# Performance work log

Measured on AMD Instinct MI355X. Metric: run time of the kernel, lower is better.

The kernel has to match this reference:

```python
import jax, jax.numpy as jnp
import numpy as np

B, T, D_IN, H, D_OUT = 64, 512, 256, 1024, 256


def _gru_cell(x, h, Wi, Wh, bi, bh):
    # x: [B, in_dim], h: [B, H]; Wi: [3H, in_dim], Wh: [3H, H]
    gi = x @ Wi.T + bi  # [B, 3H]
    gh = h @ Wh.T + bh  # [B, 3H]
    i_r, i_z, i_n = jnp.split(gi, 3, axis=-1)
    h_r, h_z, h_n = jnp.split(gh, 3, axis=-1)
    r = jax.nn.sigmoid(i_r + h_r)
    z = jax.nn.sigmoid(i_z + h_z)
    n = jnp.tanh(i_n + r * h_n)
    return (1.0 - z) * n + z * h


def setup_inputs() -> dict:
    key = jax.random.key(0)
    ks = jax.random.split(key, 11)
    s_in = 1.0 / np.sqrt(D_IN)
    s_h = 1.0 / np.sqrt(H)
    return {
        "x": jax.random.normal(ks[0], (B, T, D_IN), jnp.float32),
        "Wi0": jax.random.normal(ks[1], (3 * H, D_IN), jnp.float32) * s_in,
        "Wh0": jax.random.normal(ks[2], (3 * H, H), jnp.float32) * s_h,
        "bi0": jax.random.normal(ks[3], (3 * H,), jnp.float32) * s_h,
        "bh0": jax.random.normal(ks[4], (3 * H,), jnp.float32) * s_h,
        "Wi1": jax.random.normal(ks[5], (3 * H, H), jnp.float32) * s_h,
        "Wh1": jax.random.normal(ks[6], (3 * H, H), jnp.float32) * s_h,
        "bi1": jax.random.normal(ks[7], (3 * H,), jnp.float32) * s_h,
        "bh1": jax.random.normal(ks[8], (3 * H,), jnp.float32) * s_h,
        "Wo": jax.random.normal(ks[9], (D_OUT, H), jnp.float32) * s_h,
        "bo": jax.random.normal(ks[10], (D_OUT,), jnp.float32) * s_h,
    }


def reference(x, Wi0, Wh0, bi0, bh0, Wi1, Wh1, bi1, bh1, Wo, bo):
    b = x.shape[0]
    h0 = jnp.zeros((b, H), x.dtype)
    h1 = jnp.zeros((b, H), x.dtype)

    def step(carry, x_t):
        h0, h1 = carry
        h0 = _gru_cell(x_t, h0, Wi0, Wh0, bi0, bh0)
        h1 = _gru_cell(h0, h1, Wi1, Wh1, bi1, bh1)
        return (h0, h1), None

    (h0, h1), _ = jax.lax.scan(step, (h0, h1), jnp.swapaxes(x, 0, 1))
    return h1 @ Wo.T + bo  # [B, D_OUT]
```

## Files before the change

### kernel.cpp

```cpp
#include <hip/hip_runtime.h>

constexpr int kB    = 64;
constexpr int kT    = 512;
constexpr int kDin  = 256;
constexpr int kH    = 1024;
constexpr int kH3   = 3072;
constexpr int kDout = 256;
constexpr int kHB   = kB * kH;

typedef float  f32x4  __attribute__((ext_vector_type(4)));
typedef __bf16 bf16x8 __attribute__((ext_vector_type(8)));
typedef unsigned u32x4 __attribute__((ext_vector_type(4)));
typedef unsigned long long u64;

__device__ __forceinline__ float b2f(unsigned short u) {
  union { float f; unsigned u32; } c; c.u32 = ((unsigned)u) << 16; return c.f;
}
__device__ __forceinline__ unsigned short f2b(float f) {
  union { float f; unsigned u32; } c; c.f = f;
  unsigned r = c.u32 + 0x7fffu + ((c.u32 >> 16) & 1u);
  return (unsigned short)(r >> 16);
}
__device__ __forceinline__ bf16x8 ld8(const unsigned short* p) {
  return *reinterpret_cast<const bf16x8*>(p);
}
__device__ __forceinline__ u64 ald(const u64* p) {
  return __hip_atomic_load(p, __ATOMIC_RELAXED, __HIP_MEMORY_SCOPE_AGENT);
}
__device__ __forceinline__ unsigned ald32(const unsigned* p) {
  return __hip_atomic_load(p, __ATOMIC_RELAXED, __HIP_MEMORY_SCOPE_AGENT);
}
__device__ __forceinline__ void ast32(unsigned* p, unsigned v) {
  __hip_atomic_store(p, v, __ATOMIC_RELAXED, __HIP_MEMORY_SCOPE_AGENT);
}
__device__ __forceinline__ float sigm_(float x) { return 1.f / (1.f + __expf(-x)); }
__device__ __forceinline__ float tanh_(float x) {
  return 1.f - 2.f / (__expf(2.f * x) + 1.f);
}

#define MFMA16(a, b, c) __builtin_amdgcn_mfma_f32_16x16x32_bf16((a), (b), (c), 0, 0, 0)

__device__ __forceinline__ int swzcol(int C, int quad) {
  return (C & ~63) + ((quad ^ (((C >> 3) ^ (C >> 6)) & 7)) << 3);
}

__device__ __forceinline__ void stage_seg(unsigned short* ldsrow,
                                          const unsigned short* src, int s,
                                          int rmode) {
  if (rmode) {
    u32x4 d[8];
#pragma unroll
    for (int i = 0; i < 8; ++i) d[i] = *(const u32x4*)(src + i * 8);
#pragma unroll
    for (int i = 0; i < 8; ++i)
      *(u32x4*)&ldsrow[s * 64 + ((i ^ s) & 7) * 8] = d[i];
  } else {
    u64 w[16];
#pragma unroll
    for (int i = 0; i < 16; ++i) w[i] = ald((const u64*)src + i);
#pragma unroll
    for (int i = 0; i < 16; ++i)
      *(u64*)&ldsrow[s * 64 + (((i >> 1) ^ s) & 7) * 8 + (i & 1) * 4] = w[i];
  }
}

__device__ __forceinline__ void stage_half(unsigned short (*hl)[1032],
                                           const unsigned short* rbase,
                                           int kh, int lane, int rmode) {
  const int r = lane >> 2;
  const int s = kh * 8 + (lane & 3) * 2;
  const unsigned short* src = rbase + (size_t)r * kH + s * 64;
  stage_seg(hl[r], src, s, rmode);
  stage_seg(hl[r], src + 64, s + 1, rmode);
}

__device__ __forceinline__ void pb_post(unsigned* p, unsigned v, int lane) {
  if (lane == 0)
    __hip_atomic_store(p, v, __ATOMIC_RELEASE, __HIP_MEMORY_SCOPE_WORKGROUP);
}
__device__ __forceinline__ void pb_wait(unsigned* p, unsigned v) {
  while (__hip_atomic_load(p, __ATOMIC_ACQUIRE, __HIP_MEMORY_SCOPE_WORKGROUP) < v)
    __builtin_amdgcn_s_sleep(1);
}

__global__ void gru_prep(const float* __restrict__ x,
                         const float* __restrict__ Wi0, const float* __restrict__ Wh0,
                         const float* __restrict__ bi0, const float* __restrict__ bh0,
                         const float* __restrict__ Wi1, const float* __restrict__ Wh1,
                         const float* __restrict__ bi1, const float* __restrict__ bh1,
                         unsigned short* __restrict__ xb,
                         unsigned short* __restrict__ wi0b, unsigned short* __restrict__ wh0b,
                         unsigned short* __restrict__ wi1b, unsigned short* __restrict__ wh1b,
                         unsigned short* __restrict__ r0, unsigned short* __restrict__ r1,
                         float* __restrict__ bias, unsigned* __restrict__ sync) {
  const int stride = gridDim.x * blockDim.x;
  const int g = blockIdx.x * blockDim.x + threadIdx.x;
  for (int i = g; i < kH3 * kDin; i += stride) wi0b[i] = f2b(Wi0[i]);
  for (int i = g; i < kH3 * kH; i += stride) {
    wh0b[i] = f2b(Wh0[i]); wi1b[i] = f2b(Wi1[i]); wh1b[i] = f2b(Wh1[i]);
  }
  for (int i = g; i < kB * kT * kDin; i += stride) xb[i] = f2b(x[i]);
  for (int i = g; i < kHB; i += stride) { r0[i] = 0; r1[i] = 0; }
  for (int i = g; i < kH; i += stride) {
    bias[0 * kH + i] = bi0[0 * kH + i] + bh0[0 * kH + i];
    bias[1 * kH + i] = bi0[1 * kH + i] + bh0[1 * kH + i];
    bias[2 * kH + i] = bi0[2 * kH + i];
    bias[3 * kH + i] = bh0[2 * kH + i];
    bias[4 * kH + i] = bi1[0 * kH + i] + bh1[0 * kH + i];
    bias[5 * kH + i] = bi1[1 * kH + i] + bh1[1 * kH + i];
    bias[6 * kH + i] = bi1[2 * kH + i];
    bias[7 * kH + i] = bh1[2 * kH + i];
  }
  for (int i = g; i < 4096; i += stride) sync[i] = 0;
}

__global__ void __launch_bounds__(256, 1) gru_main(
    const unsigned short* __restrict__ xb,
    const unsigned short* __restrict__ wi0, const unsigned short* __restrict__ wh0,
    const unsigned short* __restrict__ wi1, const unsigned short* __restrict__ wh1,
    const float* __restrict__ bias,
    unsigned short* __restrict__ r0, unsigned short* __restrict__ r1,
    unsigned* __restrict__ sync, const int rmode,
    const float* __restrict__ Wo, const float* __restrict__ bo,
    float* __restrict__ out) {
  __shared__ unsigned short hl0[16][1032];
  __shared__ unsigned short hl1[16][1032];
  __shared__ float red[2][4][64][5];
  __shared__ bf16x8 wlds[2][32][64];
  __shared__ unsigned pb[8];

  const int tid  = threadIdx.x;
  const int lane = tid & 63;
  const int wv   = tid >> 6;
  const int ln15 = lane & 15;
  const int quad = lane >> 4;

  const int xcd   = blockIdx.x & 7;
  const int rest  = blockIdx.x >> 3;
  const int jsub  = rest & 7;
  const int mtile = rest >> 3;
  const int pidx  = xcd * 8 + jsub;

  const int layer = wv >> 1;
  const int kh    = wv & 1;
  const int jrow  = xcd * 128 + jsub * 16 + ln15;
  const int jcol  = jrow;

  const unsigned short *pw_r, *pw_z, *pw_n, *pv_r, *pv_z, *pv_n;
  if (layer == 0) {
    pw_r = wh0 + (size_t)(0 * kH + jrow) * kH + kh * 512 + quad * 8;
    pw_z = wh0 + (size_t)(1 * kH + jrow) * kH + kh * 512 + quad * 8;
    pw_n = wh0 + (size_t)(2 * kH + jrow) * kH + kh * 512 + quad * 8;
    pv_r = wi0 + (size_t)(0 * kH + jrow) * kDin + kh * 128 + quad * 8;
    pv_z = wi0 + (size_t)(1 * kH + jrow) * kDin + kh * 128 + quad * 8;
    pv_n = wi0 + (size_t)(2 * kH + jrow) * kDin + kh * 128 + quad * 8;
  } else {
    pw_r = wh1 + (size_t)(0 * kH + jrow) * kH + kh * 512 + quad * 8;
    pw_z = wh1 + (size_t)(1 * kH + jrow) * kH + kh * 512 + quad * 8;
    pw_n = wh1 + (size_t)(2 * kH + jrow) * kH + kh * 512 + quad * 8;
    pv_r = wi1 + (size_t)(0 * kH + jrow) * kH + kh * 512 + quad * 8;
    pv_z = wi1 + (size_t)(1 * kH + jrow) * kH + kh * 512 + quad * 8;
    pv_n = wi1 + (size_t)(2 * kH + jrow) * kH + kh * 512 + quad * 8;
  }

  const float* bb = bias + layer * 4 * kH;
  const float b_r = bb[jcol];
  const float b_z = bb[kH + jcol];
  const float b_i = bb[2 * kH + jcol];
  const float b_h = bb[3 * kH + jcol];

  bf16x8 W[64];
  if (layer == 0) {
#pragma unroll
    for (int kk = 0; kk < 16; ++kk) {
      W[kk]      = ld8(pw_r + kk * 32);
      W[16 + kk] = ld8(pw_z + kk * 32);
      W[32 + kk] = ld8(pw_n + kk * 32);
    }
#pragma unroll
    for (int kk = 0; kk < 4; ++kk) {
      W[48 + kk] = ld8(pv_r + kk * 32);
      W[52 + kk] = ld8(pv_z + kk * 32);
      W[56 + kk] = ld8(pv_n + kk * 32);
    }
  } else {
#pragma unroll
    for (int kk = 0; kk < 16; ++kk) {
      W[kk]      = ld8(pv_r + kk * 32);
      W[16 + kk] = ld8(pv_z + kk * 32);
      W[32 + kk] = ld8(pv_n + kk * 32);
      W[48 + kk] = ld8(pw_r + kk * 32);
      wlds[kh][kk][lane]      = ld8(pw_z + kk * 32);
      wlds[kh][16 + kk][lane] = ld8(pw_n + kk * 32);
    }
  }

  if (tid < 8) pb[tid] = 0;
  __syncthreads();

  const f32x4 z4 = {0.f, 0.f, 0.f, 0.f};
  unsigned* fl0 = sync + (size_t)xcd * 512 + mtile * 64;
  unsigned* fl1 = sync + (size_t)xcd * 512 + 256 + mtile * 64;

  float hprev[4] = {0.f, 0.f, 0.f, 0.f};

  for (int t = 0; t <= kT; ++t) {
    const bool l0c = (t < kT);
    const bool l1c = (t >= 1);
    const int s0r = rmode ? t : (t & 1);
    const int s0w = rmode ? (t + 1) : ((t + 1) & 1);
    const int s1r = rmode ? (t >= 1 ? t - 1 : 0) : ((t >= 1 ? t - 1 : 0) & 1);
    const int s1w = rmode ? t : (t & 1);

    const unsigned short* r0base = r0 + (size_t)s0r * kHB + (size_t)(mtile * 16) * kH;
    const unsigned short* r1base = r1 + (size_t)s1r * kHB + (size_t)(mtile * 16) * kH;
    const int kb = kh * 512;

    if (layer == 0) {
      f32x4 a_r = z4, a_z = z4, a_i = z4, a_h = z4;
      if (l0c) {
        const unsigned short* xp = xb + (size_t)(mtile * 16 + ln15) * (kT * kDin) +
                                   t * kDin + kh * 128 + quad * 8;
        bf16x8 xa[4];
#pragma unroll
        for (int i = 0; i < 4; ++i) xa[i] = ld8(xp + i * 32);
#pragma unroll
        for (int kk = 0; kk < 4; ++kk) {
          a_r = MFMA16(xa[kk], W[48 + kk], a_r);
          a_z = MFMA16(xa[kk], W[52 + kk], a_z);
          a_i = MFMA16(xa[kk], W[56 + kk], a_i);
        }
      }
      {
        int first = 1;
        for (;;) {
          bool ok;
          if (rmode) {
            int a = (int)ald32(fl0 + kh * 32 + (lane & 31));
            ok = __all(a >= t);
          } else {
            int a = (int)ald32(fl0 + lane);
            int b = (int)ald32(fl1 + lane);
            ok = __all(a >= t && b >= t - 1);
          }
          if (ok) break;
          if (first) { __builtin_amdgcn_s_sleep(8); first = 0; }
          else       { __builtin_amdgcn_s_sleep(2); }
        }
      }
      pb_wait(&pb[2 + kh], t);
      stage_half(hl0, r0base, kh, lane, rmode);
      pb_post(&pb[0 + kh], t + 1, lane);
      if (l0c) {
#pragma unroll
        for (int kk = 0; kk < 16; ++kk) {
          bf16x8 A = *(const bf16x8*)&hl0[ln15][swzcol(kb + kk * 32, quad)];
          a_r = MFMA16(A, W[kk], a_r);
          a_z = MFMA16(A, W[16 + kk], a_z);
          a_h = MFMA16(A, W[32 + kk], a_h);
        }
      }
      if (kh == 0) {
        pb_wait(&pb[4], t + 1);
        if (l0c) {
          float hv4[4];
#pragma unroll
          for (int q = 0; q < 4; ++q) {
            float sr = a_r[q] + red[0][0][lane][q];
            float sz = a_z[q] + red[0][1][lane][q];
            float si = a_i[q] + red[0][2][lane][q];
            float sh = a_h[q] + red[0][3][lane][q];
            float rg = sigm_(sr + b_r);
            float zg = sigm_(sz + b_z);
            float ng = tanh_(si + b_i + rg * (sh + b_h));
            hv4[q] = (1.f - zg) * ng + zg * hprev[q];
            hprev[q] = hv4[q];
          }
          unsigned short* dst = r0 + (size_t)s0w * kHB;
#pragma unroll
          for (int q = 0; q < 4; ++q) {
            float pv = __shfl_xor(hv4[q], 1);
            if (!(lane & 1)) {
              unsigned pk = (unsigned)f2b(hv4[q]) | ((unsigned)f2b(pv) << 16);
              ast32((unsigned*)(dst + (size_t)(mtile * 16 + quad * 4 + q) * kH +
                                (jcol & ~1)),
                    pk);
            }
          }
          asm volatile("s_waitcnt vmcnt(0)" ::: "memory");
          if (lane < 8) ast32(sync + lane * 512 + mtile * 64 + pidx, (unsigned)(t + 1));
        }
        pb_post(&pb[6], t + 1, lane);
      } else {
        pb_wait(&pb[6], t);
        if (l0c) {
#pragma unroll
          for (int q = 0; q < 4; ++q) {
            red[0][0][lane][q] = a_r[q]; red[0][1][lane][q] = a_z[q];
            red[0][2][lane][q] = a_i[q]; red[0][3][lane][q] = a_h[q];
          }
        }
        pb_post(&pb[4], t + 1, lane);
      }
    } else {
      {
        int first = 1;
        for (;;) {
          bool ok;
          if (rmode) {
            int a = (int)ald32(fl0 + kh * 32 + (lane & 31));
            int b = (int)ald32(fl1 + kh * 32 + (lane & 31));
            ok = __all(a >= t && b >= t - 1);
          } else {
            int a = (int)ald32(fl0 + lane);
            int b = (int)ald32(fl1 + lane);
            ok = __all(a >= t && b >= t - 1);
          }
          if (ok) break;
          if (first) { __builtin_amdgcn_s_sleep(8); first = 0; }
          else       { __builtin_amdgcn_s_sleep(2); }
        }
      }
      stage_half(hl1, r1base, kh, lane, rmode);
      pb_wait(&pb[0 + kh], t + 1);
      f32x4 a_r = z4, a_z = z4, a_i = z4, a_h = z4;
      if (l1c) {
#pragma unroll
        for (int kk = 0; kk < 16; ++kk) {
          bf16x8 A0 = *(const bf16x8*)&hl0[ln15][swzcol(kb + kk * 32, quad)];
          a_r = MFMA16(A0, W[kk], a_r);
          a_z = MFMA16(A0, W[16 + kk], a_z);
          a_i = MFMA16(A0, W[32 + kk], a_i);
          bf16x8 A1 = *(const bf16x8*)&hl1[ln15][swzcol(kb + kk * 32, quad)];
          a_r = MFMA16(A1, W[48 + kk], a_r);
          a_z = MFMA16(A1, wlds[kh][kk][lane], a_z);
          a_h = MFMA16(A1, wlds[kh][16 + kk][lane], a_h);
        }
      }
      pb_post(&pb[2 + kh], t + 1, lane);
      if (kh == 0) {
        pb_wait(&pb[5], t + 1);
        if (l1c) {
          float hv4[4];
#pragma unroll
          for (int q = 0; q < 4; ++q) {
            float sr = a_r[q] + red[1][0][lane][q];
            float sz = a_z[q] + red[1][1][lane][q];
            float si = a_i[q] + red[1][2][lane][q];
            float sh = a_h[q] + red[1][3][lane][q];
            float rg = sigm_(sr + b_r);
            float zg = sigm_(sz + b_z);
            float ng = tanh_(si + b_i + rg * (sh + b_h));
            hv4[q] = (1.f - zg) * ng + zg * hprev[q];
            hprev[q] = hv4[q];
          }
          unsigned short* dst = r1 + (size_t)s1w * kHB;
#pragma unroll
          for (int q = 0; q < 4; ++q) {
            float pv = __shfl_xor(hv4[q], 1);
            if (!(lane & 1)) {
              unsigned pk = (unsigned)f2b(hv4[q]) | ((unsigned)f2b(pv) << 16);
              ast32((unsigned*)(dst + (size_t)(mtile * 16 + quad * 4 + q) * kH +
                                (jcol & ~1)),
                    pk);
            }
          }
          asm volatile("s_waitcnt vmcnt(0)" ::: "memory");
          if (lane < 8)
            ast32(sync + lane * 512 + 256 + mtile * 64 + pidx, (unsigned)t);
        }
        pb_post(&pb[7], t + 1, lane);
      } else {
        pb_wait(&pb[7], t);
        if (l1c) {
#pragma unroll
          for (int q = 0; q < 4; ++q) {
            red[1][0][lane][q] = a_r[q]; red[1][1][lane][q] = a_z[q];
            red[1][2][lane][q] = a_i[q]; red[1][3][lane][q] = a_h[q];
          }
        }
        pb_post(&pb[5], t + 1, lane);
      }
    }
  }

  if (wv == 0) {
    int first = 1;
    for (;;) {
      int f = (int)ald32(fl1 + lane);
      if (__all(f >= (int)kT)) break;
      if (first) { __builtin_amdgcn_s_sleep(8); first = 0; }
      else       { __builtin_amdgcn_s_sleep(2); }
    }
  }
  __syncthreads();
  {
    const int sfin = rmode ? kT : 0;
    const int r = tid >> 4, s = tid & 15;
    const unsigned short* b1 =
        r1 + (size_t)sfin * kHB + (size_t)(mtile * 16 + r) * kH + s * 64;
    if (rmode) {
      u32x4 d[8];
#pragma unroll
      for (int i = 0; i < 8; ++i) d[i] = *(const u32x4*)(b1 + i * 8);
#pragma unroll
      for (int i = 0; i < 8; ++i) *(u32x4*)&hl0[r][s * 64 + i * 8] = d[i];
    } else {
      u64 w[16];
#pragma unroll
      for (int i = 0; i < 16; ++i) w[i] = ald((const u64*)b1 + i);
#pragma unroll
      for (int i = 0; i < 16; ++i) *(u64*)&hl0[r][s * 64 + i * 4] = w[i];
    }
  }
  __syncthreads();
  {
    const int c  = tid & 31;
    const int rr = tid >> 5;
    const int col = jsub * 32 + c;
    const float* wr = Wo + (size_t)col * kH;
    float acc0 = bo[col], acc1 = bo[col];
#pragma unroll 8
    for (int k = 0; k < kH; k += 4) {
      float4 w4 = *reinterpret_cast<const float4*>(wr + k);
      acc0 += b2f(hl0[rr][k]) * w4.x + b2f(hl0[rr][k + 1]) * w4.y +
              b2f(hl0[rr][k + 2]) * w4.z + b2f(hl0[rr][k + 3]) * w4.w;
      acc1 += b2f(hl0[rr + 8][k]) * w4.x + b2f(hl0[rr + 8][k + 1]) * w4.y +
              b2f(hl0[rr + 8][k + 2]) * w4.z + b2f(hl0[rr + 8][k + 3]) * w4.w;
    }
    out[(mtile * 16 + rr) * kDout + col] = acc0;
    out[(mtile * 16 + rr + 8) * kDout + col] = acc1;
  }
}

extern "C" void kernel_launch(void* const* d_in, const int* in_sizes, int n_in,
                              void* d_out, int out_size, void* d_ws, size_t ws_size,
                              hipStream_t stream) {
  const float* x   = (const float*)d_in[0];
  const float* Wi0 = (const float*)d_in[1];
  const float* Wh0 = (const float*)d_in[2];
  const float* bi0 = (const float*)d_in[3];
  const float* bh0 = (const float*)d_in[4];
  const float* Wi1 = (const float*)d_in[5];
  const float* Wh1 = (const float*)d_in[6];
  const float* bi1 = (const float*)d_in[7];
  const float* bh1 = (const float*)d_in[8];
  const float* Wo  = (const float*)d_in[9];
  const float* bo  = (const float*)d_in[10];

  char* ws = (char*)d_ws;
  size_t off = 0;
  auto take = [&](size_t bytes) {
    size_t r = off;
    off += (bytes + 255) & ~(size_t)255;
    return r;
  };
  unsigned short* xb   = (unsigned short*)(ws + take((size_t)kB * kT * kDin * 2));
  unsigned short* wi0b = (unsigned short*)(ws + take((size_t)kH3 * kDin * 2));
  unsigned short* wh0b = (unsigned short*)(ws + take((size_t)kH3 * kH * 2));
  unsigned short* wi1b = (unsigned short*)(ws + take((size_t)kH3 * kH * 2));
  unsigned short* wh1b = (unsigned short*)(ws + take((size_t)kH3 * kH * 2));
  float*          bias = (float*)(ws + take(8 * kH * sizeof(float)));
  unsigned*       sync = (unsigned*)(ws + take(4096 * sizeof(unsigned)));

  const size_t slot_b = (size_t)kHB * 2;
  int rmode = 1;
  size_t ring_slots = (size_t)kT + 1;
  if (off + 2 * (ring_slots * slot_b) + (1u << 20) > ws_size) {
    rmode = 0;
    ring_slots = 2;
  }
  unsigned short* r0 = (unsigned short*)(ws + take(ring_slots * slot_b));
  unsigned short* r1 = (unsigned short*)(ws + take(ring_slots * slot_b));

  gru_prep<<<2048, 256, 0, stream>>>(x, Wi0, Wh0, bi0, bh0, Wi1, Wh1, bi1, bh1,
                                     xb, wi0b, wh0b, wi1b, wh1b, r0, r1, bias,
                                     sync);
  gru_main<<<256, 256, 0, stream>>>(xb, wi0b, wh0b, wi1b, wh1b, bias, r0, r1,
                                    sync, rmode, Wo, bo, (float*)d_out);
}
```

Measured before the change: 3.288 ms.

## Give each layer its own h0 LDS copy and drop cross-layer workgroup barriers

The layer-0 and layer-1 waves previously shared one staged h0 buffer in LDS and coordinated through pb flags around the staging. Now layer-1 waves stage their own copy of h0 (hl0B), so the staging handshake flags go away. Part of the layer-1 z-gate weights moves from LDS into registers (W2), and the LDS rows are unpadded and XOR-swizzled by row to avoid bank conflicts. The cost is extra global/L2 traffic for the duplicated h0 staging and higher register pressure.

```diff
diff --git a/kernel.cpp b/kernel.cpp
--- a/kernel.cpp
+++ b/kernel.cpp
@@ -40,38 +40,38 @@
 
 #define MFMA16(a, b, c) __builtin_amdgcn_mfma_f32_16x16x32_bf16((a), (b), (c), 0, 0, 0)
 
-__device__ __forceinline__ int swzcol(int C, int quad) {
-  return (C & ~63) + ((quad ^ (((C >> 3) ^ (C >> 6)) & 7)) << 3);
+__device__ __forceinline__ int swz(int C, int quad, int row) {
+  return (C & ~63) + (((quad ^ ((C >> 3) ^ (C >> 6)) ^ row) & 7) << 3);
 }
 
 __device__ __forceinline__ void stage_seg(unsigned short* ldsrow,
                                           const unsigned short* src, int s,
-                                          int rmode) {
+                                          int r, int rmode) {
   if (rmode) {
     u32x4 d[8];
 #pragma unroll
     for (int i = 0; i < 8; ++i) d[i] = *(const u32x4*)(src + i * 8);
 #pragma unroll
     for (int i = 0; i < 8; ++i)
-      *(u32x4*)&ldsrow[s * 64 + ((i ^ s) & 7) * 8] = d[i];
+      *(u32x4*)&ldsrow[s * 64 + ((i ^ s ^ r) & 7) * 8] = d[i];
   } else {
     u64 w[16];
 #pragma unroll
     for (int i = 0; i < 16; ++i) w[i] = ald((const u64*)src + i);
 #pragma unroll
     for (int i = 0; i < 16; ++i)
-      *(u64*)&ldsrow[s * 64 + (((i >> 1) ^ s) & 7) * 8 + (i & 1) * 4] = w[i];
-  }
-}
-
-__device__ __forceinline__ void stage_half(unsigned short (*hl)[1032],
+      *(u64*)&ldsrow[s * 64 + (((i >> 1) ^ s ^ r) & 7) * 8 + (i & 1) * 4] = w[i];
+  }
+}
+
+__device__ __forceinline__ void stage_half(unsigned short (*hl)[1024],
                                            const unsigned short* rbase,
                                            int kh, int lane, int rmode) {
   const int r = lane >> 2;
   const int s = kh * 8 + (lane & 3) * 2;
   const unsigned short* src = rbase + (size_t)r * kH + s * 64;
-  stage_seg(hl[r], src, s, rmode);
-  stage_seg(hl[r], src + 64, s + 1, rmode);
+  stage_seg(hl[r], src, s, r, rmode);
+  stage_seg(hl[r], src + 64, s + 1, r, rmode);
 }
 
 __device__ __forceinline__ void pb_post(unsigned* p, unsigned v, int lane) {
@@ -123,11 +123,12 @@
     unsigned* __restrict__ sync, const int rmode,
     const float* __restrict__ Wo, const float* __restrict__ bo,
     float* __restrict__ out) {
-  __shared__ unsigned short hl0[16][1032];
-  __shared__ unsigned short hl1[16][1032];
+  __shared__ unsigned short hl0A[16][1024];
+  __shared__ unsigned short hl0B[16][1024];
+  __shared__ unsigned short hl1v[16][1024];
   __shared__ float red[2][4][64][5];
-  __shared__ bf16x8 wlds[2][32][64];
-  __shared__ unsigned pb[8];
+  __shared__ bf16x8 wlds[2][16][64];
+  __shared__ unsigned pb[4];
 
   const int tid  = threadIdx.x;
   const int lane = tid & 63;
@@ -169,7 +170,7 @@
   const float b_i = bb[2 * kH + jcol];
   const float b_h = bb[3 * kH + jcol];
 
-  bf16x8 W[64];
+  bf16x8 W[64], W2[16];
   if (layer == 0) {
 #pragma unroll
     for (int kk = 0; kk < 16; ++kk) {
@@ -190,12 +191,12 @@
       W[16 + kk] = ld8(pv_z + kk * 32);
       W[32 + kk] = ld8(pv_n + kk * 32);
       W[48 + kk] = ld8(pw_r + kk * 32);
-      wlds[kh][kk][lane]      = ld8(pw_z + kk * 32);
-      wlds[kh][16 + kk][lane] = ld8(pw_n + kk * 32);
-    }
-  }
-
-  if (tid < 8) pb[tid] = 0;
+      W2[kk]     = ld8(pw_z + kk * 32);
+      wlds[kh][kk][lane] = ld8(pw_n + kk * 32);
+    }
+  }
+
+  if (tid < 4) pb[tid] = 0;
   __syncthreads();
 
   const f32x4 z4 = {0.f, 0.f, 0.f, 0.f};
@@ -248,20 +249,18 @@
           else       { __builtin_amdgcn_s_sleep(2); }
         }
       }
-      pb_wait(&pb[2 + kh], t);
-      stage_half(hl0, r0base, kh, lane, rmode);
-      pb_post(&pb[0 + kh], t + 1, lane);
+      stage_half(hl0A, r0base, kh, lane, rmode);
       if (l0c) {
 #pragma unroll
         for (int kk = 0; kk < 16; ++kk) {
-          bf16x8 A = *(const bf16x8*)&hl0[ln15][swzcol(kb + kk * 32, quad)];
+          bf16x8 A = *(const bf16x8*)&hl0A[ln15][swz(kb + kk * 32, quad, ln15)];
           a_r = MFMA16(A, W[kk], a_r);
           a_z = MFMA16(A, W[16 + kk], a_z);
           a_h = MFMA16(A, W[32 + kk], a_h);
         }
       }
       if (kh == 0) {
-        pb_wait(&pb[4], t + 1);
+        pb_wait(&pb[0], t + 1);
         if (l0c) {
           float hv4[4];
 #pragma unroll
@@ -288,11 +287,12 @@
             }
           }
           asm volatile("s_waitcnt vmcnt(0)" ::: "memory");
-          if (lane < 8) ast32(sync + lane * 512 + mtile * 64 + pidx, (unsigned)(t + 1));
-        }
-        pb_post(&pb[6], t + 1, lane);
+          if (lane < 8)
+            ast32(sync + lane * 512 + mtile * 64 + pidx, (unsigned)(t + 1));
+        }
+        pb_post(&pb[1], t + 1, lane);
       } else {
-        pb_wait(&pb[6], t);
+        pb_wait(&pb[1], t);
         if (l0c) {
 #pragma unroll
           for (int q = 0; q < 4; ++q) {
@@ -300,7 +300,7 @@
             red[0][2][lane][q] = a_i[q]; red[0][3][lane][q] = a_h[q];
           }
         }
-        pb_post(&pb[4], t + 1, lane);
+        pb_post(&pb[0], t + 1, lane);
       }
     } else {
       {
@@ -321,25 +321,24 @@
           else       { __builtin_amdgcn_s_sleep(2); }
         }
       }
-      stage_half(hl1, r1base, kh, lane, rmode);
-      pb_wait(&pb[0 + kh], t + 1);
+      stage_half(hl0B, r0base, kh, lane, rmode);
+      stage_half(hl1v, r1base, kh, lane, rmode);
       f32x4 a_r = z4, a_z = z4, a_i = z4, a_h = z4;
       if (l1c) {
 #pragma unroll
         for (int kk = 0; kk < 16; ++kk) {
-          bf16x8 A0 = *(const bf16x8*)&hl0[ln15][swzcol(kb + kk * 32, quad)];
+          bf16x8 A0 = *(const bf16x8*)&hl0B[ln15][swz(kb + kk * 32, quad, ln15)];
           a_r = MFMA16(A0, W[kk], a_r);
           a_z = MFMA16(A0, W[16 + kk], a_z);
           a_i = MFMA16(A0, W[32 + kk], a_i);
-          bf16x8 A1 = *(const bf16x8*)&hl1[ln15][swzcol(kb + kk * 32, quad)];
+          bf16x8 A1 = *(const bf16x8*)&hl1v[ln15][swz(kb + kk * 32, quad, ln15)];
           a_r = MFMA16(A1, W[48 + kk], a_r);
-          a_z = MFMA16(A1, wlds[kh][kk][lane], a_z);
-          a_h = MFMA16(A1, wlds[kh][16 + kk][lane], a_h);
-        }
-      }
-      pb_post(&pb[2 + kh], t + 1, lane);
+          a_z = MFMA16(A1, W2[kk], a_z);
+          a_h = MFMA16(A1, wlds[kh][kk][lane], a_h);
+        }
+      }
       if (kh == 0) {
-        pb_wait(&pb[5], t + 1);
+        pb_wait(&pb[2], t + 1);
         if (l1c) {
           float hv4[4];
 #pragma unroll
@@ -369,9 +368,9 @@
           if (lane < 8)
             ast32(sync + lane * 512 + 256 + mtile * 64 + pidx, (unsigned)t);
         }
-        pb_post(&pb[7], t + 1, lane);
+        pb_post(&pb[3], t + 1, lane);
       } else {
-        pb_wait(&pb[7], t);
+        pb_wait(&pb[3], t);
         if (l1c) {
 #pragma unroll
           for (int q = 0; q < 4; ++q) {
@@ -379,7 +378,7 @@
             red[1][2][lane][q] = a_i[q]; red[1][3][lane][q] = a_h[q];
           }
         }
-        pb_post(&pb[5], t + 1, lane);
+        pb_post(&pb[2], t + 1, lane);
       }
     }
   }
@@ -404,13 +403,13 @@
 #pragma unroll
       for (int i = 0; i < 8; ++i) d[i] = *(const u32x4*)(b1 + i * 8);
 #pragma unroll
-      for (int i = 0; i < 8; ++i) *(u32x4*)&hl0[r][s * 64 + i * 8] = d[i];
+      for (int i = 0; i < 8; ++i) *(u32x4*)&hl0A[r][s * 64 + i * 8] = d[i];
     } else {
       u64 w[16];
 #pragma unroll
       for (int i = 0; i < 16; ++i) w[i] = ald((const u64*)b1 + i);
 #pragma unroll
-      for (int i = 0; i < 16; ++i) *(u64*)&hl0[r][s * 64 + i * 4] = w[i];
+      for (int i = 0; i < 16; ++i) *(u64*)&hl0A[r][s * 64 + i * 4] = w[i];
     }
   }
   __syncthreads();
@@ -423,10 +422,10 @@
 #pragma unroll 8
     for (int k = 0; k < kH; k += 4) {
       float4 w4 = *reinterpret_cast<const float4*>(wr + k);
-      acc0 += b2f(hl0[rr][k]) * w4.x + b2f(hl0[rr][k + 1]) * w4.y +
-              b2f(hl0[rr][k + 2]) * w4.z + b2f(hl0[rr][k + 3]) * w4.w;
-      acc1 += b2f(hl0[rr + 8][k]) * w4.x + b2f(hl0[rr + 8][k + 1]) * w4.y +
-              b2f(hl0[rr + 8][k + 2]) * w4.z + b2f(hl0[rr + 8][k + 3]) * w4.w;
+      acc0 += b2f(hl0A[rr][k]) * w4.x + b2f(hl0A[rr][k + 1]) * w4.y +
+              b2f(hl0A[rr][k + 2]) * w4.z + b2f(hl0A[rr][k + 3]) * w4.w;
+      acc1 += b2f(hl0A[rr + 8][k]) * w4.x + b2f(hl0A[rr + 8][k + 1]) * w4.y +
+              b2f(hl0A[rr + 8][k + 2]) * w4.z + b2f(hl0A[rr + 8][k + 3]) * w4.w;
     }
     out[(mtile * 16 + rr) * kDout + col] = acc0;
     out[(mtile * 16 + rr + 8) * kDout + col] = acc1;
```

Result: slower. 4.892 ms (+48.8%).
